# Kernel optimization log

Hardware: AMD Instinct MI355X
Metric: run time of the kernel (lower is better)

Reference implementation:

```python
import jax, jax.numpy as jnp
import numpy as np
from jax.ops import segment_sum, segment_max

N_NODES = 16384
N_EDGES = 262144
NODE_DIM = 480
HIDDEN = 256
OUT_DIM = 128
HEADS = 4
N_GRAPHS = 256


def setup_inputs() -> dict:
    key = jax.random.key(0)
    ks = jax.random.split(key, 40)
    p = {}
    p['x'] = jax.random.normal(ks[0], (N_NODES, NODE_DIM), jnp.float32)
    p['edge_index'] = jax.random.randint(ks[1], (2, N_EDGES), 0, N_NODES)
    p['edge_attr'] = jax.random.uniform(ks[2], (N_EDGES, 1), dtype=jnp.float32)
    p['batch'] = jnp.sort(jax.random.randint(ks[3], (N_NODES,), 0, N_GRAPHS))
    p['num_graphs'] = N_GRAPHS
    def w(k, shape):
        return jax.random.normal(k, shape, jnp.float32) * 0.05
    i = 4
    for l, (din, h, c) in zip((1, 2, 3), [(NODE_DIM, HEADS, HIDDEN // HEADS), (HIDDEN, HEADS, HIDDEN // HEADS), (HIDDEN, 1, OUT_DIM)]):
        dout = h * c
        p[f'Wl{l}'] = w(ks[i], (din, dout)); i += 1
        p[f'bl{l}'] = jnp.zeros((dout,), jnp.float32)
        p[f'Wr{l}'] = w(ks[i], (din, dout)); i += 1
        p[f'br{l}'] = jnp.zeros((dout,), jnp.float32)
        p[f'We{l}'] = w(ks[i], (1, dout)); i += 1
        p[f'att{l}'] = w(ks[i], (h, c)); i += 1
        p[f'bo{l}'] = jnp.zeros((dout,), jnp.float32)
    for l, d in [(1, HIDDEN), (2, HIDDEN), (3, OUT_DIM)]:
        p[f'g{l}'] = jnp.ones((d,), jnp.float32)
        p[f'b{l}'] = jnp.zeros((d,), jnp.float32)
    p['Wres'] = w(ks[i], (NODE_DIM, HIDDEN))
    return p


def _layer_norm(x, g, b):
    mu = x.mean(-1, keepdims=True)
    v = ((x - mu) ** 2).mean(-1, keepdims=True)
    return (x - mu) * jax.lax.rsqrt(v + 1e-5) * g + b


def _gatv2(x, src, dst, ea, Wl, bl, Wr, br, We, att, bias):
    # PyG GATv2Conv, eval mode (dropout off), add_self_loops=True, fill_value='mean'
    N = x.shape[0]
    H, C = att.shape
    # self-loop edge attr = scatter-mean of incoming edge attrs per node
    deg = segment_sum(jnp.ones((src.shape[0],), x.dtype), dst, num_segments=N)
    loop_ea = segment_sum(ea, dst, num_segments=N) / jnp.maximum(deg, 1.0)[:, None]
    ar = jnp.arange(N, dtype=src.dtype)
    src2 = jnp.concatenate([src, ar])
    dst2 = jnp.concatenate([dst, ar])
    ea2 = jnp.concatenate([ea, loop_ea], axis=0)
    xl = (x @ Wl + bl).reshape(N, H, C)
    xr = (x @ Wr + br).reshape(N, H, C)
    e = (ea2 @ We).reshape(-1, H, C)
    m = jax.nn.leaky_relu(xl[src2] + xr[dst2] + e, 0.2)  # [E', H, C]
    alpha = jnp.einsum('ehc,hc->eh', m, att)
    amax = segment_max(alpha, dst2, num_segments=N)  # [N, H]; every node has a self loop
    ex = jnp.exp(alpha - amax[dst2])
    denom = segment_sum(ex, dst2, num_segments=N)
    a = ex / denom[dst2]
    out = segment_sum(a[:, :, None] * xl[src2], dst2, num_segments=N)  # [N, H, C]
    return out.reshape(N, H * C) + bias


def _forward(x, edge_attr, params, edge_index, batch, num_graphs):
    (Wl1, bl1, Wr1, br1, We1, att1, bo1,
     Wl2, bl2, Wr2, br2, We2, att2, bo2,
     Wl3, bl3, Wr3, br3, We3, att3, bo3,
     g1, b1, g2, b2, g3, b3, Wres) = params
    src, dst = edge_index[0], edge_index[1]
    gelu = lambda t: jax.nn.gelu(t, approximate=False)
    h = gelu(_layer_norm(_gatv2(x, src, dst, edge_attr, Wl1, bl1, Wr1, br1, We1, att1, bo1), g1, b1))
    h = h + x @ Wres
    h2 = gelu(_layer_norm(_gatv2(h, src, dst, edge_attr, Wl2, bl2, Wr2, br2, We2, att2, bo2), g2, b2))
    h2 = h2 + h
    h3 = _layer_norm(_gatv2(h2, src, dst, edge_attr, Wl3, bl3, Wr3, br3, We3, att3, bo3), g3, b3)
    # global mean pool over graphs
    sums = segment_sum(h3, batch, num_segments=num_graphs)
    cnt = segment_sum(jnp.ones((h3.shape[0],), h3.dtype), batch, num_segments=num_graphs)
    return sums / jnp.maximum(cnt, 1.0)[:, None]


def reference(x, edge_index, edge_attr, batch, num_graphs,
              Wl1, bl1, Wr1, br1, We1, att1, bo1,
              Wl2, bl2, Wr2, br2, We2, att2, bo2,
              Wl3, bl3, Wr3, br3, We3, att3, bo3,
              g1, b1, g2, b2, g3, b3, Wres):
    params = (Wl1, bl1, Wr1, br1, We1, att1, bo1,
              Wl2, bl2, Wr2, br2, We2, att2, bo2,
              Wl3, bl3, Wr3, br3, We3, att3, bo3,
              g1, b1, g2, b2, g3, b3, Wres)
    return _forward(x, edge_attr, params, edge_index, batch, num_graphs)
```

## Files before the change

kernel.cpp:

```cpp
#include <hip/hip_runtime.h>
#include <hip/hip_bf16.h>
#include <math.h>

#define NN 16384
#define NE 262144
#define KDIM1 480
#define DHID 256
#define DOUT3 128
#define NG 256

typedef short bf16x8 __attribute__((ext_vector_type(8)));
typedef float f32x4 __attribute__((ext_vector_type(4)));

#define LOG2E 1.44269504088896340736f

__device__ __forceinline__ unsigned short f2bf(float f) {
  unsigned u = __float_as_uint(f);
  unsigned r = (u + 0x7fffu + ((u >> 16) & 1u)) >> 16;
  return (unsigned short)r;
}
__device__ __forceinline__ float bf2f(unsigned short u) {
  return __uint_as_float((unsigned)u << 16);
}

__device__ __forceinline__ void gload_lds16(const void* g, void* l) {
  __builtin_amdgcn_global_load_lds((const __attribute__((address_space(1))) void*)g,
                                   (__attribute__((address_space(3))) void*)l,
                                   16, 0, 0);
}


__global__ __launch_bounds__(256) void k_edge_count(const int* __restrict__ ei,
                                                    const float* __restrict__ ea,
                                                    int* __restrict__ deg,
                                                    float* __restrict__ easum) {
  int e = blockIdx.x * 256 + threadIdx.x;
  if (e >= NE) return;
  int d = ei[NE + e];
  atomicAdd(&deg[d], 1);
  atomicAdd(&easum[d], ea[e]);
}

__global__ __launch_bounds__(1024) void k_scan(const int* __restrict__ deg,
                                               float* __restrict__ easum,
                                               int* __restrict__ offs,
                                               int* __restrict__ cursor) {
  __shared__ int sums[1024];
  int t = threadIdx.x;
  int base = t * 16;
  int local[16];
  int s = 0;
#pragma unroll
  for (int i = 0; i < 16; ++i) { local[i] = deg[base + i]; s += local[i]; }
  sums[t] = s;
  __syncthreads();
  for (int d = 1; d < 1024; d <<= 1) {
    int v = (t >= d) ? sums[t - d] : 0;
    __syncthreads();
    sums[t] += v;
    __syncthreads();
  }
  int prefix = (t == 0) ? 0 : sums[t - 1];
#pragma unroll
  for (int i = 0; i < 16; ++i) {
    offs[base + i] = prefix;
    cursor[base + i] = prefix;
    prefix += local[i];
  }
  if (t == 1023) offs[NN] = prefix;
#pragma unroll
  for (int i = 0; i < 16; ++i) {
    easum[base + i] = easum[base + i] / fmaxf((float)local[i], 1.f);
  }
}

__global__ __launch_bounds__(256) void k_fill_csr(const int* __restrict__ ei,
                                                  const float* __restrict__ ea,
                                                  int* __restrict__ cursor,
                                                  int* __restrict__ csr_src,
                                                  float* __restrict__ csr_ea) {
  int e = blockIdx.x * 256 + threadIdx.x;
  if (e >= NE) return;
  int s = ei[e];
  int d = ei[NE + e];
  int pos = atomicAdd(&cursor[d], 1);
  csr_src[pos] = s;
  csr_ea[pos] = ea[e];
}


__global__ __launch_bounds__(256) void k_f32_to_bf16(const float* __restrict__ in,
                                                     unsigned short* __restrict__ out,
                                                     int n) {
  int i = (blockIdx.x * 256 + threadIdx.x) * 4;
  if (i >= n) return;
  float4 v = *(const float4*)&in[i];
  ushort4 o;
  o.x = f2bf(v.x); o.y = f2bf(v.y); o.z = f2bf(v.z); o.w = f2bf(v.w);
  *(ushort4*)&out[i] = o;
}

__global__ __launch_bounds__(256) void k_transpose_bf16(const float* __restrict__ W,
                                                        unsigned short* __restrict__ Wt,
                                                        int K, int N) {
  int idx = blockIdx.x * 256 + threadIdx.x;
  if (idx >= K * N) return;
  int n = idx / K, k = idx % K;
  Wt[idx] = f2bf(W[(size_t)k * N + n]);
}

__global__ __launch_bounds__(256) void k_transpose_lr(const float* __restrict__ Wl,
                                                      const float* __restrict__ Wr,
                                                      unsigned short* __restrict__ Wt,
                                                      int K, int NH) {
  int idx = blockIdx.x * 256 + threadIdx.x;
  if (idx >= 2 * NH * K) return;
  int n = idx / K, k = idx % K;
  float v = (n < NH) ? Wl[(size_t)k * NH + n] : Wr[(size_t)k * NH + (n - NH)];
  Wt[idx] = f2bf(v);
}


#define GEMM_CORE128(A_, Bt_, K_)                                                \
  __shared__ short As[128 * 32];                                                 \
  __shared__ short Bs[128 * 32];                                                 \
  int t = threadIdx.x;                                                           \
  int w = t >> 6;                                                                \
  int lane = t & 63;                                                             \
  int bm = blockIdx.y * 128;                                                     \
  int bn = blockIdx.x * 128;                                                     \
  int wr = w >> 1, wc = w & 1;                                                   \
               \
  const short* Ag0 = A_ + (size_t)(bm + w * 16 + (lane >> 2)) * K_ + (lane & 3) * 8;        \
  const short* Ag1 = A_ + (size_t)(bm + 64 + w * 16 + (lane >> 2)) * K_ + (lane & 3) * 8;   \
  const short* Bg0 = Bt_ + (size_t)(bn + w * 16 + (lane >> 2)) * K_ + (lane & 3) * 8;       \
  const short* Bg1 = Bt_ + (size_t)(bn + 64 + w * 16 + (lane >> 2)) * K_ + (lane & 3) * 8;  \
  short* Al0 = &As[w * 16 * 32];                                                 \
  short* Al1 = &As[(64 + w * 16) * 32];                                          \
  short* Bl0 = &Bs[w * 16 * 32];                                                 \
  short* Bl1 = &Bs[(64 + w * 16) * 32];                                          \
  f32x4 acc[4][4] = {};                                                          \
  for (int k0 = 0; k0 < K_; k0 += 32) {                                          \
    gload_lds16(Ag0, Al0);                                                       \
    gload_lds16(Ag1, Al1);                                                       \
    gload_lds16(Bg0, Bl0);                                                       \
    gload_lds16(Bg1, Bl1);                                                       \
    Ag0 += 32; Ag1 += 32; Bg0 += 32; Bg1 += 32;                                  \
    __syncthreads();                                                             \
    bf16x8 af[4], bf[4];                                                         \
    _Pragma("unroll")                                                            \
    for (int mi = 0; mi < 4; ++mi)                                               \
      af[mi] = *(const bf16x8*)&As[(wr * 64 + mi * 16 + (lane & 15)) * 32 + (lane >> 4) * 8]; \
    _Pragma("unroll")                                                            \
    for (int ni = 0; ni < 4; ++ni)                                               \
      bf[ni] = *(const bf16x8*)&Bs[(wc * 64 + ni * 16 + (lane & 15)) * 32 + (lane >> 4) * 8]; \
    _Pragma("unroll")                                                            \
    for (int mi = 0; mi < 4; ++mi)                                               \
      _Pragma("unroll")                                                          \
      for (int ni = 0; ni < 4; ++ni)                                             \
        acc[mi][ni] = __builtin_amdgcn_mfma_f32_16x16x32_bf16(af[mi], bf[ni], acc[mi][ni], 0, 0, 0); \
    __syncthreads();                                                             \
  }                                                                              \
  int col = lane & 15;                                                           \
  int row4 = (lane >> 4) * 4;

__global__ __launch_bounds__(256) void gemm_lr(const short* __restrict__ A,
                                               const short* __restrict__ Wt,
                                               const float* __restrict__ bl,
                                               const float* __restrict__ br,
                                               unsigned short* __restrict__ xlb,
                                               unsigned short* __restrict__ xrb,
                                               int K, int NH) {
  GEMM_CORE128(A, Wt, K)
  bool right = (bn >= NH);
  unsigned short* outp = right ? xrb : xlb;
  const float* bias = right ? br : bl;
  int cbase = right ? bn - NH : bn;
#pragma unroll
  for (int mi = 0; mi < 4; ++mi) {
#pragma unroll
    for (int ni = 0; ni < 4; ++ni) {
      f32x4 a = acc[mi][ni];
      int gc = cbase + wc * 64 + ni * 16 + col;
      float bv = bias[gc];
#pragma unroll
      for (int r = 0; r < 4; ++r) {
        int gr = bm + wr * 64 + mi * 16 + row4 + r;
        outp[(size_t)gr * NH + gc] = f2bf(a[r] + bv);
      }
    }
  }
}

__global__ __launch_bounds__(256) void gemm_res(const short* __restrict__ A,
                                                const short* __restrict__ Wt,
                                                float* __restrict__ Cf,
                                                unsigned short* __restrict__ outb,
                                                int K, int N) {
  GEMM_CORE128(A, Wt, K)
#pragma unroll
  for (int mi = 0; mi < 4; ++mi) {
#pragma unroll
    for (int ni = 0; ni < 4; ++ni) {
      f32x4 a = acc[mi][ni];
      int gc = bn + wc * 64 + ni * 16 + col;
#pragma unroll
      for (int r = 0; r < 4; ++r) {
        int gr = bm + wr * 64 + mi * 16 + row4 + r;
        size_t o = (size_t)gr * N + gc;
        float v = a[r] + Cf[o];
        Cf[o] = v;
        outb[o] = f2bf(v);
      }
    }
  }
}


template<int D, int H, bool GELU_, bool RES_, bool WF32, bool WBF16>
__global__ __launch_bounds__(256) void gat_fused(
    const unsigned short* __restrict__ xlb, const unsigned short* __restrict__ xrb,
    const float* __restrict__ We, const float* __restrict__ att,
    const float* __restrict__ bo,
    const int* __restrict__ offs, const int* __restrict__ csr_src,
    const float* __restrict__ csr_ea, const float* __restrict__ loop_ea,
    const float* __restrict__ g, const float* __restrict__ bln,
    const float* __restrict__ res,
    float* __restrict__ outf, unsigned short* __restrict__ outb) {
  constexpr int P = D / 64;
  constexpr int C = D / H;
  constexpr int GROUP = C / P;
  int n = (blockIdx.x * blockDim.x + threadIdx.x) >> 6;
  int lane = threadIdx.x & 63;
  if (n >= NN) return;
  int d0 = lane * P;

  float xrv[P], wev[P], attv[P];
  if constexpr (P == 4) {
    ushort4 u = *(const ushort4*)&xrb[(size_t)n * D + d0];
    xrv[0] = bf2f(u.x); xrv[1] = bf2f(u.y); xrv[2] = bf2f(u.z); xrv[3] = bf2f(u.w);
    *(float4*)wev = *(const float4*)&We[d0];
    *(float4*)attv = *(const float4*)&att[d0];
  } else {
    ushort2 u = *(const ushort2*)&xrb[(size_t)n * D + d0];
    xrv[0] = bf2f(u.x); xrv[1] = bf2f(u.y);
    *(float2*)wev = *(const float2*)&We[d0];
    *(float2*)attv = *(const float2*)&att[d0];
  }
#pragma unroll
  for (int p = 0; p < P; ++p) attv[p] *= LOG2E;

#define GATHER(dst, srcidx)                                                  \
  {                                                                          \
    if constexpr (P == 4) {                                                  \
      ushort4 u_ = *(const ushort4*)&xlb[(size_t)(srcidx) * D + d0];         \
      dst[0] = bf2f(u_.x); dst[1] = bf2f(u_.y);                              \
      dst[2] = bf2f(u_.z); dst[3] = bf2f(u_.w);                              \
    } else {                                                                 \
      ushort2 u_ = *(const ushort2*)&xlb[(size_t)(srcidx) * D + d0];         \
      dst[0] = bf2f(u_.x); dst[1] = bf2f(u_.y);                              \
    }                                                                        \
  }

#define ALPHA(out_, xv_, eav_)                                               \
  {                                                                          \
    float partial_ = 0.f;                                                    \
    _Pragma("unroll")                                                        \
    for (int p = 0; p < P; ++p) {                                            \
      float s_ = xv_[p] + xrv[p] + (eav_) * wev[p];                          \
      s_ = fmaxf(s_, 0.2f * s_);                                             \
      partial_ = fmaf(s_, attv[p], partial_);                                \
    }                                                                        \
    _Pragma("unroll")                                                        \
    for (int w_ = 1; w_ < GROUP; w_ <<= 1) partial_ += __shfl_xor(partial_, w_, 64); \
    out_ = partial_;                                                         \
  }

  float acc[P];
  float xs[P];
  GATHER(xs, n)
  float m;
  ALPHA(m, xs, loop_ea[n])
  float l = 1.f;
#pragma unroll
  for (int p = 0; p < P; ++p) acc[p] = xs[p];

  int beg = offs[n];
  int cnt = offs[n + 1] - beg;
  int sbeg = __builtin_amdgcn_readfirstlane(beg);
  int scnt = __builtin_amdgcn_readfirstlane(cnt);

  int e = 0;
  for (; e + 2 <= scnt; e += 2) {
    int src0 = csr_src[sbeg + e];
    int src1 = csr_src[sbeg + e + 1];
    float ea0 = csr_ea[sbeg + e];
    float ea1 = csr_ea[sbeg + e + 1];
    float xv0[P], xv1[P];
    GATHER(xv0, src0)
    GATHER(xv1, src1)
    float a0, a1;
    ALPHA(a0, xv0, ea0)
    ALPHA(a1, xv1, ea1)
    float nm = fmaxf(m, fmaxf(a0, a1));
    float sc = exp2f(m - nm);
    float pe0 = exp2f(a0 - nm);
    float pe1 = exp2f(a1 - nm);
    l = fmaf(l, sc, pe0 + pe1);
#pragma unroll
    for (int p = 0; p < P; ++p)
      acc[p] = fmaf(acc[p], sc, fmaf(pe0, xv0[p], pe1 * xv1[p]));
    m = nm;
  }
  if (e < scnt) {
    int src0 = csr_src[sbeg + e];
    float ea0 = csr_ea[sbeg + e];
    float xv0[P];
    GATHER(xv0, src0)
    float a0;
    ALPHA(a0, xv0, ea0)
    float nm = fmaxf(m, a0);
    float sc = exp2f(m - nm);
    float pe0 = exp2f(a0 - nm);
    l = fmaf(l, sc, pe0);
#pragma unroll
    for (int p = 0; p < P; ++p) acc[p] = fmaf(acc[p], sc, pe0 * xv0[p]);
    m = nm;
  }
#undef GATHER
#undef ALPHA

  float inv = 1.f / l;
  float y[P];
#pragma unroll
  for (int p = 0; p < P; ++p) y[p] = fmaf(acc[p], inv, bo[d0 + p]);

  float s = 0.f, s2 = 0.f;
#pragma unroll
  for (int p = 0; p < P; ++p) { s += y[p]; s2 = fmaf(y[p], y[p], s2); }
#pragma unroll
  for (int w = 1; w < 64; w <<= 1) {
    s += __shfl_xor(s, w, 64);
    s2 += __shfl_xor(s2, w, 64);
  }
  float mu = s * (1.f / D);
  float var = s2 * (1.f / D) - mu * mu;
  float rr = rsqrtf(var + 1e-5f);

  float z[P];
#pragma unroll
  for (int p = 0; p < P; ++p) {
    float v = (y[p] - mu) * rr * g[d0 + p] + bln[d0 + p];
    if (GELU_) v = 0.5f * v * (1.f + erff(v * 0.70710678118654752f));
    if (RES_) v += res[(size_t)n * D + d0 + p];
    z[p] = v;
  }
  if (WF32) {
    float* orow = outf + (size_t)n * D;
    if constexpr (P == 4) *(float4*)&orow[d0] = *(float4*)z;
    else                  *(float2*)&orow[d0] = *(float2*)z;
  }
  if (WBF16) {
    unsigned short* orow = outb + (size_t)n * D;
    if constexpr (P == 4) {
      ushort4 o; o.x = f2bf(z[0]); o.y = f2bf(z[1]); o.z = f2bf(z[2]); o.w = f2bf(z[3]);
      *(ushort4*)&orow[d0] = o;
    } else {
      ushort2 o; o.x = f2bf(z[0]); o.y = f2bf(z[1]);
      *(ushort2*)&orow[d0] = o;
    }
  }
}


__device__ __forceinline__ int lower_bound_i(const int* arr, int n, int val) {
  int lo = 0, hi = n;
  while (lo < hi) {
    int mid = (lo + hi) >> 1;
    if (arr[mid] < val) lo = mid + 1; else hi = mid;
  }
  return lo;
}

__global__ __launch_bounds__(128) void k_pool(const float* __restrict__ h3,
                                              const int* __restrict__ batch,
                                              float* __restrict__ out) {
  int gidx = blockIdx.x;
  int d = threadIdx.x;
  int lo = lower_bound_i(batch, NN, gidx);
  int hi = lower_bound_i(batch, NN, gidx + 1);
  float s = 0.f;
  for (int n = lo; n < hi; ++n) s += h3[(size_t)n * DOUT3 + d];
  int cnt = hi - lo;
  out[gidx * DOUT3 + d] = s / fmaxf((float)cnt, 1.f);
}


extern "C" void kernel_launch(void* const* d_in, const int* in_sizes, int n_in,
                              void* d_out, int out_size, void* d_ws, size_t ws_size,
                              hipStream_t stream) {
  const float* x   = (const float*)d_in[0];
  const int*   ei  = (const int*)d_in[1];
  const float* ea  = (const float*)d_in[2];
  const int*   bat = (const int*)d_in[3];
  const float* Wl1 = (const float*)d_in[5];  const float* bl1 = (const float*)d_in[6];
  const float* Wr1 = (const float*)d_in[7];  const float* br1 = (const float*)d_in[8];
  const float* We1 = (const float*)d_in[9];  const float* at1 = (const float*)d_in[10];
  const float* bo1 = (const float*)d_in[11];
  const float* Wl2 = (const float*)d_in[12]; const float* bl2 = (const float*)d_in[13];
  const float* Wr2 = (const float*)d_in[14]; const float* br2 = (const float*)d_in[15];
  const float* We2 = (const float*)d_in[16]; const float* at2 = (const float*)d_in[17];
  const float* bo2 = (const float*)d_in[18];
  const float* Wl3 = (const float*)d_in[19]; const float* bl3 = (const float*)d_in[20];
  const float* Wr3 = (const float*)d_in[21]; const float* br3 = (const float*)d_in[22];
  const float* We3 = (const float*)d_in[23]; const float* at3 = (const float*)d_in[24];
  const float* bo3 = (const float*)d_in[25];
  const float* g1 = (const float*)d_in[26]; const float* b1 = (const float*)d_in[27];
  const float* g2 = (const float*)d_in[28]; const float* b2 = (const float*)d_in[29];
  const float* g3 = (const float*)d_in[30]; const float* b3 = (const float*)d_in[31];
  const float* Wres = (const float*)d_in[32];
  float* out = (float*)d_out;

  char* ws = (char*)d_ws;
  size_t off = 0;
  unsigned short* xlb = (unsigned short*)(ws + off); off += (size_t)NN * DHID * 2;
  unsigned short* xrb = (unsigned short*)(ws + off); off += (size_t)NN * DHID * 2;
  float* hb = (float*)(ws + off); off += (size_t)NN * DHID * 4;
  float* h3 = (float*)(ws + off); off += (size_t)NN * DOUT3 * 4;
  unsigned short* actb0 = (unsigned short*)(ws + off); off += (size_t)NN * KDIM1 * 2;
  unsigned short* actb1 = (unsigned short*)(ws + off); off += (size_t)NN * DHID * 2;
  int*   deg    = (int*)(ws + off); off += NN * 4;
  int*   offs   = (int*)(ws + off); off += (NN + 1) * 4 + 60;
  int*   cursor = (int*)(ws + off); off += NN * 4;
  float* easum  = (float*)(ws + off); off += NN * 4;
  int*   csr_src = (int*)(ws + off); off += (size_t)NE * 4;
  float* csr_ea  = (float*)(ws + off); off += (size_t)NE * 4;
  unsigned short* Wc1 = (unsigned short*)(ws + off); off += (size_t)2 * DHID * KDIM1 * 2;
  unsigned short* Wrs = (unsigned short*)(ws + off); off += (size_t)DHID * KDIM1 * 2;
  unsigned short* Wc2 = (unsigned short*)(ws + off); off += (size_t)2 * DHID * DHID * 2;
  unsigned short* Wc3 = (unsigned short*)(ws + off); off += (size_t)2 * DOUT3 * DHID * 2;

  hipMemsetAsync(deg, 0, NN * 4, stream);
  hipMemsetAsync(easum, 0, NN * 4, stream);
  k_edge_count<<<NE / 256, 256, 0, stream>>>(ei, ea, deg, easum);
  k_scan<<<1, 1024, 0, stream>>>(deg, easum, offs, cursor);
  k_fill_csr<<<NE / 256, 256, 0, stream>>>(ei, ea, cursor, csr_src, csr_ea);

  k_f32_to_bf16<<<(NN * KDIM1 / 4 + 255) / 256, 256, 0, stream>>>(x, actb0, NN * KDIM1);
  k_transpose_lr<<<(2 * DHID * KDIM1 + 255) / 256, 256, 0, stream>>>(Wl1, Wr1, Wc1, KDIM1, DHID);
  k_transpose_bf16<<<(DHID * KDIM1 + 255) / 256, 256, 0, stream>>>(Wres, Wrs, KDIM1, DHID);
  k_transpose_lr<<<(2 * DHID * DHID + 255) / 256, 256, 0, stream>>>(Wl2, Wr2, Wc2, DHID, DHID);
  k_transpose_lr<<<(2 * DOUT3 * DHID + 255) / 256, 256, 0, stream>>>(Wl3, Wr3, Wc3, DHID, DOUT3);

  dim3 blk(256);
  int nwave_blocks = NN / 4;

  gemm_lr<<<dim3(2 * DHID / 128, NN / 128), blk, 0, stream>>>(
      (const short*)actb0, (const short*)Wc1, bl1, br1, xlb, xrb, KDIM1, DHID);
  gat_fused<DHID, 4, true, false, true, false><<<nwave_blocks, blk, 0, stream>>>(
      xlb, xrb, We1, at1, bo1, offs, csr_src, csr_ea, easum, g1, b1, nullptr, hb, nullptr);
  gemm_res<<<dim3(DHID / 128, NN / 128), blk, 0, stream>>>(
      (const short*)actb0, (const short*)Wrs, hb, actb1, KDIM1, DHID);

  gemm_lr<<<dim3(2 * DHID / 128, NN / 128), blk, 0, stream>>>(
      (const short*)actb1, (const short*)Wc2, bl2, br2, xlb, xrb, DHID, DHID);
  gat_fused<DHID, 4, true, true, false, true><<<nwave_blocks, blk, 0, stream>>>(
      xlb, xrb, We2, at2, bo2, offs, csr_src, csr_ea, easum, g2, b2, hb, nullptr, actb1);

  gemm_lr<<<dim3(2 * DOUT3 / 128, NN / 128), blk, 0, stream>>>(
      (const short*)actb1, (const short*)Wc3, bl3, br3, xlb, xrb, DHID, DOUT3);
  gat_fused<DOUT3, 1, false, false, true, false><<<nwave_blocks, blk, 0, stream>>>(
      xlb, xrb, We3, at3, bo3, offs, csr_src, csr_ea, easum, g3, b3, nullptr, h3, nullptr);

  k_pool<<<NG, 128, 0, stream>>>(h3, bat, out);
}
```

Measured before the change: 274.7 us.

## Use persistent atomic work queue in GAT kernels, unroll edges by four, fuse prep kernels

The GAT aggregation kernels become persistent: 2048 blocks pull node indices from a global atomic counter instead of launching one wave per node, which is meant to balance the uneven per-node degrees. The edge loop is unrolled from two to four edges per iteration to keep more gathers in flight. The five input conversion and weight-transpose kernels are merged into one prep launch, and the two memsets become one that also clears the queue counters. The trade-off is one atomic per node and coarser tail behaviour.

```diff
diff --git a/kernel.cpp b/kernel.cpp
--- a/kernel.cpp
+++ b/kernel.cpp
@@ -89,35 +89,57 @@
 }
 
 
-__global__ __launch_bounds__(256) void k_f32_to_bf16(const float* __restrict__ in,
-                                                     unsigned short* __restrict__ out,
-                                                     int n) {
-  int i = (blockIdx.x * 256 + threadIdx.x) * 4;
-  if (i >= n) return;
-  float4 v = *(const float4*)&in[i];
-  ushort4 o;
-  o.x = f2bf(v.x); o.y = f2bf(v.y); o.z = f2bf(v.z); o.w = f2bf(v.w);
-  *(ushort4*)&out[i] = o;
-}
-
-__global__ __launch_bounds__(256) void k_transpose_bf16(const float* __restrict__ W,
-                                                        unsigned short* __restrict__ Wt,
-                                                        int K, int N) {
+#define PREP_S0 (NN * KDIM1 / 4)
+#define PREP_S1 (2 * DHID * KDIM1)
+#define PREP_S2 (DHID * KDIM1)
+#define PREP_S3 (2 * DHID * DHID)
+#define PREP_S4 (2 * DOUT3 * DHID)
+#define PREP_TOTAL (PREP_S0 + PREP_S1 + PREP_S2 + PREP_S3 + PREP_S4)
+
+__global__ __launch_bounds__(256) void k_prep(
+    const float* __restrict__ x,
+    const float* __restrict__ Wl1, const float* __restrict__ Wr1,
+    const float* __restrict__ Wres,
+    const float* __restrict__ Wl2, const float* __restrict__ Wr2,
+    const float* __restrict__ Wl3, const float* __restrict__ Wr3,
+    unsigned short* __restrict__ actb0, unsigned short* __restrict__ Wc1,
+    unsigned short* __restrict__ Wrs, unsigned short* __restrict__ Wc2,
+    unsigned short* __restrict__ Wc3) {
   int idx = blockIdx.x * 256 + threadIdx.x;
-  if (idx >= K * N) return;
-  int n = idx / K, k = idx % K;
-  Wt[idx] = f2bf(W[(size_t)k * N + n]);
-}
-
-__global__ __launch_bounds__(256) void k_transpose_lr(const float* __restrict__ Wl,
-                                                      const float* __restrict__ Wr,
-                                                      unsigned short* __restrict__ Wt,
-                                                      int K, int NH) {
-  int idx = blockIdx.x * 256 + threadIdx.x;
-  if (idx >= 2 * NH * K) return;
-  int n = idx / K, k = idx % K;
-  float v = (n < NH) ? Wl[(size_t)k * NH + n] : Wr[(size_t)k * NH + (n - NH)];
-  Wt[idx] = f2bf(v);
+  if (idx < PREP_S0) {
+    int i = idx * 4;
+    float4 v = *(const float4*)&x[i];
+    ushort4 o;
+    o.x = f2bf(v.x); o.y = f2bf(v.y); o.z = f2bf(v.z); o.w = f2bf(v.w);
+    *(ushort4*)&actb0[i] = o;
+    return;
+  }
+  idx -= PREP_S0;
+  if (idx < PREP_S1) {
+    int n = idx / KDIM1, k = idx % KDIM1;
+    float v = (n < DHID) ? Wl1[(size_t)k * DHID + n] : Wr1[(size_t)k * DHID + (n - DHID)];
+    Wc1[idx] = f2bf(v);
+    return;
+  }
+  idx -= PREP_S1;
+  if (idx < PREP_S2) {
+    int n = idx / KDIM1, k = idx % KDIM1;
+    Wrs[idx] = f2bf(Wres[(size_t)k * DHID + n]);
+    return;
+  }
+  idx -= PREP_S2;
+  if (idx < PREP_S3) {
+    int n = idx / DHID, k = idx % DHID;
+    float v = (n < DHID) ? Wl2[(size_t)k * DHID + n] : Wr2[(size_t)k * DHID + (n - DHID)];
+    Wc2[idx] = f2bf(v);
+    return;
+  }
+  idx -= PREP_S3;
+  if (idx < PREP_S4) {
+    int n = idx / DHID, k = idx % DHID;
+    float v = (n < DOUT3) ? Wl3[(size_t)k * DOUT3 + n] : Wr3[(size_t)k * DOUT3 + (n - DOUT3)];
+    Wc3[idx] = f2bf(v);
+  }
 }
 
 
@@ -130,7 +152,6 @@
   int bm = blockIdx.y * 128;                                                     \
   int bn = blockIdx.x * 128;                                                     \
   int wr = w >> 1, wc = w & 1;                                                   \
-               \
   const short* Ag0 = A_ + (size_t)(bm + w * 16 + (lane >> 2)) * K_ + (lane & 3) * 8;        \
   const short* Ag1 = A_ + (size_t)(bm + 64 + w * 16 + (lane >> 2)) * K_ + (lane & 3) * 8;   \
   const short* Bg0 = Bt_ + (size_t)(bn + w * 16 + (lane >> 2)) * K_ + (lane & 3) * 8;       \
@@ -147,18 +168,18 @@
     gload_lds16(Bg1, Bl1);                                                       \
     Ag0 += 32; Ag1 += 32; Bg0 += 32; Bg1 += 32;                                  \
     __syncthreads();                                                             \
-    bf16x8 af[4], bf[4];                                                         \
+    bf16x8 af[4], bfv[4];                                                        \
     _Pragma("unroll")                                                            \
     for (int mi = 0; mi < 4; ++mi)                                               \
       af[mi] = *(const bf16x8*)&As[(wr * 64 + mi * 16 + (lane & 15)) * 32 + (lane >> 4) * 8]; \
     _Pragma("unroll")                                                            \
     for (int ni = 0; ni < 4; ++ni)                                               \
-      bf[ni] = *(const bf16x8*)&Bs[(wc * 64 + ni * 16 + (lane & 15)) * 32 + (lane >> 4) * 8]; \
+      bfv[ni] = *(const bf16x8*)&Bs[(wc * 64 + ni * 16 + (lane & 15)) * 32 + (lane >> 4) * 8]; \
     _Pragma("unroll")                                                            \
     for (int mi = 0; mi < 4; ++mi)                                               \
       _Pragma("unroll")                                                          \
       for (int ni = 0; ni < 4; ++ni)                                             \
-        acc[mi][ni] = __builtin_amdgcn_mfma_f32_16x16x32_bf16(af[mi], bf[ni], acc[mi][ni], 0, 0, 0); \
+        acc[mi][ni] = __builtin_amdgcn_mfma_f32_16x16x32_bf16(af[mi], bfv[ni], acc[mi][ni], 0, 0, 0); \
     __syncthreads();                                                             \
   }                                                                              \
   int col = lane & 15;                                                           \
@@ -226,24 +247,19 @@
     const float* __restrict__ csr_ea, const float* __restrict__ loop_ea,
     const float* __restrict__ g, const float* __restrict__ bln,
     const float* __restrict__ res,
-    float* __restrict__ outf, unsigned short* __restrict__ outb) {
+    float* __restrict__ outf, unsigned short* __restrict__ outb,
+    int* __restrict__ gcnt) {
   constexpr int P = D / 64;
   constexpr int C = D / H;
   constexpr int GROUP = C / P;
-  int n = (blockIdx.x * blockDim.x + threadIdx.x) >> 6;
   int lane = threadIdx.x & 63;
-  if (n >= NN) return;
   int d0 = lane * P;
 
-  float xrv[P], wev[P], attv[P];
+  float wev[P], attv[P];
   if constexpr (P == 4) {
-    ushort4 u = *(const ushort4*)&xrb[(size_t)n * D + d0];
-    xrv[0] = bf2f(u.x); xrv[1] = bf2f(u.y); xrv[2] = bf2f(u.z); xrv[3] = bf2f(u.w);
     *(float4*)wev = *(const float4*)&We[d0];
     *(float4*)attv = *(const float4*)&att[d0];
   } else {
-    ushort2 u = *(const ushort2*)&xrb[(size_t)n * D + d0];
-    xrv[0] = bf2f(u.x); xrv[1] = bf2f(u.y);
     *(float2*)wev = *(const float2*)&We[d0];
     *(float2*)attv = *(const float2*)&att[d0];
   }
@@ -276,100 +292,127 @@
     out_ = partial_;                                                         \
   }
 
-  float acc[P];
-  float xs[P];
-  GATHER(xs, n)
-  float m;
-  ALPHA(m, xs, loop_ea[n])
-  float l = 1.f;
-#pragma unroll
-  for (int p = 0; p < P; ++p) acc[p] = xs[p];
-
-  int beg = offs[n];
-  int cnt = offs[n + 1] - beg;
-  int sbeg = __builtin_amdgcn_readfirstlane(beg);
-  int scnt = __builtin_amdgcn_readfirstlane(cnt);
-
-  int e = 0;
-  for (; e + 2 <= scnt; e += 2) {
-    int src0 = csr_src[sbeg + e];
-    int src1 = csr_src[sbeg + e + 1];
-    float ea0 = csr_ea[sbeg + e];
-    float ea1 = csr_ea[sbeg + e + 1];
-    float xv0[P], xv1[P];
-    GATHER(xv0, src0)
-    GATHER(xv1, src1)
-    float a0, a1;
-    ALPHA(a0, xv0, ea0)
-    ALPHA(a1, xv1, ea1)
-    float nm = fmaxf(m, fmaxf(a0, a1));
-    float sc = exp2f(m - nm);
-    float pe0 = exp2f(a0 - nm);
-    float pe1 = exp2f(a1 - nm);
-    l = fmaf(l, sc, pe0 + pe1);
-#pragma unroll
-    for (int p = 0; p < P; ++p)
-      acc[p] = fmaf(acc[p], sc, fmaf(pe0, xv0[p], pe1 * xv1[p]));
-    m = nm;
-  }
-  if (e < scnt) {
-    int src0 = csr_src[sbeg + e];
-    float ea0 = csr_ea[sbeg + e];
-    float xv0[P];
-    GATHER(xv0, src0)
-    float a0;
-    ALPHA(a0, xv0, ea0)
-    float nm = fmaxf(m, a0);
-    float sc = exp2f(m - nm);
-    float pe0 = exp2f(a0 - nm);
-    l = fmaf(l, sc, pe0);
-#pragma unroll
-    for (int p = 0; p < P; ++p) acc[p] = fmaf(acc[p], sc, pe0 * xv0[p]);
-    m = nm;
+  for (;;) {
+    int n;
+    if (lane == 0) n = atomicAdd(gcnt, 1);
+    n = __shfl(n, 0, 64);
+    if (n >= NN) break;
+
+    float xrv[P];
+    if constexpr (P == 4) {
+      ushort4 u = *(const ushort4*)&xrb[(size_t)n * D + d0];
+      xrv[0] = bf2f(u.x); xrv[1] = bf2f(u.y); xrv[2] = bf2f(u.z); xrv[3] = bf2f(u.w);
+    } else {
+      ushort2 u = *(const ushort2*)&xrb[(size_t)n * D + d0];
+      xrv[0] = bf2f(u.x); xrv[1] = bf2f(u.y);
+    }
+
+    float acc[P];
+    float xs[P];
+    GATHER(xs, n)
+    float m;
+    ALPHA(m, xs, loop_ea[n])
+    float l = 1.f;
+#pragma unroll
+    for (int p = 0; p < P; ++p) acc[p] = xs[p];
+
+    int beg = offs[n];
+    int cnt = offs[n + 1] - beg;
+    int sbeg = __builtin_amdgcn_readfirstlane(beg);
+    int scnt = __builtin_amdgcn_readfirstlane(cnt);
+
+    int e = 0;
+    for (; e + 4 <= scnt; e += 4) {
+      int src0 = csr_src[sbeg + e];
+      int src1 = csr_src[sbeg + e + 1];
+      int src2 = csr_src[sbeg + e + 2];
+      int src3 = csr_src[sbeg + e + 3];
+      float ea0 = csr_ea[sbeg + e];
+      float ea1 = csr_ea[sbeg + e + 1];
+      float ea2 = csr_ea[sbeg + e + 2];
+      float ea3 = csr_ea[sbeg + e + 3];
+      float xv0[P], xv1[P], xv2[P], xv3[P];
+      GATHER(xv0, src0)
+      GATHER(xv1, src1)
+      GATHER(xv2, src2)
+      GATHER(xv3, src3)
+      float a0, a1, a2, a3;
+      ALPHA(a0, xv0, ea0)
+      ALPHA(a1, xv1, ea1)
+      ALPHA(a2, xv2, ea2)
+      ALPHA(a3, xv3, ea3)
+      float nm = fmaxf(fmaxf(m, fmaxf(a0, a1)), fmaxf(a2, a3));
+      float sc = exp2f(m - nm);
+      float pe0 = exp2f(a0 - nm);
+      float pe1 = exp2f(a1 - nm);
+      float pe2 = exp2f(a2 - nm);
+      float pe3 = exp2f(a3 - nm);
+      l = fmaf(l, sc, (pe0 + pe1) + (pe2 + pe3));
+#pragma unroll
+      for (int p = 0; p < P; ++p)
+        acc[p] = fmaf(acc[p], sc,
+                      fmaf(pe0, xv0[p], fmaf(pe1, xv1[p], fmaf(pe2, xv2[p], pe3 * xv3[p]))));
+      m = nm;
+    }
+    for (; e < scnt; ++e) {
+      int src0 = csr_src[sbeg + e];
+      float ea0 = csr_ea[sbeg + e];
+      float xv0[P];
+      GATHER(xv0, src0)
+      float a0;
+      ALPHA(a0, xv0, ea0)
+      float nm = fmaxf(m, a0);
+      float sc = exp2f(m - nm);
+      float pe0 = exp2f(a0 - nm);
+      l = fmaf(l, sc, pe0);
+#pragma unroll
+      for (int p = 0; p < P; ++p) acc[p] = fmaf(acc[p], sc, pe0 * xv0[p]);
+      m = nm;
+    }
+
+    float inv = 1.f / l;
+    float y[P];
+#pragma unroll
+    for (int p = 0; p < P; ++p) y[p] = fmaf(acc[p], inv, bo[d0 + p]);
+
+    float s = 0.f, s2 = 0.f;
+#pragma unroll
+    for (int p = 0; p < P; ++p) { s += y[p]; s2 = fmaf(y[p], y[p], s2); }
+#pragma unroll
+    for (int w = 1; w < 64; w <<= 1) {
+      s += __shfl_xor(s, w, 64);
+      s2 += __shfl_xor(s2, w, 64);
+    }
+    float mu = s * (1.f / D);
+    float var = s2 * (1.f / D) - mu * mu;
+    float rr = rsqrtf(var + 1e-5f);
+
+    float z[P];
+#pragma unroll
+    for (int p = 0; p < P; ++p) {
+      float v = (y[p] - mu) * rr * g[d0 + p] + bln[d0 + p];
+      if (GELU_) v = 0.5f * v * (1.f + erff(v * 0.70710678118654752f));
+      if (RES_) v += res[(size_t)n * D + d0 + p];
+      z[p] = v;
+    }
+    if (WF32) {
+      float* orow = outf + (size_t)n * D;
+      if constexpr (P == 4) *(float4*)&orow[d0] = *(float4*)z;
+      else                  *(float2*)&orow[d0] = *(float2*)z;
+    }
+    if (WBF16) {
+      unsigned short* orow = outb + (size_t)n * D;
+      if constexpr (P == 4) {
+        ushort4 o; o.x = f2bf(z[0]); o.y = f2bf(z[1]); o.z = f2bf(z[2]); o.w = f2bf(z[3]);
+        *(ushort4*)&orow[d0] = o;
+      } else {
+        ushort2 o; o.x = f2bf(z[0]); o.y = f2bf(z[1]);
+        *(ushort2*)&orow[d0] = o;
+      }
+    }
   }
 #undef GATHER
 #undef ALPHA
-
-  float inv = 1.f / l;
-  float y[P];
-#pragma unroll
-  for (int p = 0; p < P; ++p) y[p] = fmaf(acc[p], inv, bo[d0 + p]);
-
-  float s = 0.f, s2 = 0.f;
-#pragma unroll
-  for (int p = 0; p < P; ++p) { s += y[p]; s2 = fmaf(y[p], y[p], s2); }
-#pragma unroll
-  for (int w = 1; w < 64; w <<= 1) {
-    s += __shfl_xor(s, w, 64);
-    s2 += __shfl_xor(s2, w, 64);
-  }
-  float mu = s * (1.f / D);
-  float var = s2 * (1.f / D) - mu * mu;
-  float rr = rsqrtf(var + 1e-5f);
-
-  float z[P];
-#pragma unroll
-  for (int p = 0; p < P; ++p) {
-    float v = (y[p] - mu) * rr * g[d0 + p] + bln[d0 + p];
-    if (GELU_) v = 0.5f * v * (1.f + erff(v * 0.70710678118654752f));
-    if (RES_) v += res[(size_t)n * D + d0 + p];
-    z[p] = v;
-  }
-  if (WF32) {
-    float* orow = outf + (size_t)n * D;
-    if constexpr (P == 4) *(float4*)&orow[d0] = *(float4*)z;
-    else                  *(float2*)&orow[d0] = *(float2*)z;
-  }
-  if (WBF16) {
-    unsigned short* orow = outb + (size_t)n * D;
-    if constexpr (P == 4) {
-      ushort4 o; o.x = f2bf(z[0]); o.y = f2bf(z[1]); o.z = f2bf(z[2]); o.w = f2bf(z[3]);
-      *(ushort4*)&orow[d0] = o;
-    } else {
-      ushort2 o; o.x = f2bf(z[0]); o.y = f2bf(z[1]);
-      *(ushort2*)&orow[d0] = o;
-    }
-  }
 }
 
 
@@ -423,16 +466,18 @@
 
   char* ws = (char*)d_ws;
   size_t off = 0;
+  int*   deg    = (int*)(ws + off); off += NN * 4;
+  float* easum  = (float*)(ws + off); off += NN * 4;
+  int*   gcnt   = (int*)(ws + off); off += 16;
+  size_t zero_bytes = off;
   unsigned short* xlb = (unsigned short*)(ws + off); off += (size_t)NN * DHID * 2;
   unsigned short* xrb = (unsigned short*)(ws + off); off += (size_t)NN * DHID * 2;
   float* hb = (float*)(ws + off); off += (size_t)NN * DHID * 4;
   float* h3 = (float*)(ws + off); off += (size_t)NN * DOUT3 * 4;
   unsigned short* actb0 = (unsigned short*)(ws + off); off += (size_t)NN * KDIM1 * 2;
   unsigned short* actb1 = (unsigned short*)(ws + off); off += (size_t)NN * DHID * 2;
-  int*   deg    = (int*)(ws + off); off += NN * 4;
   int*   offs   = (int*)(ws + off); off += (NN + 1) * 4 + 60;
   int*   cursor = (int*)(ws + off); off += NN * 4;
-  float* easum  = (float*)(ws + off); off += NN * 4;
   int*   csr_src = (int*)(ws + off); off += (size_t)NE * 4;
   float* csr_ea  = (float*)(ws + off); off += (size_t)NE * 4;
   unsigned short* Wc1 = (unsigned short*)(ws + off); off += (size_t)2 * DHID * KDIM1 * 2;
@@ -440,37 +485,32 @@
   unsigned short* Wc2 = (unsigned short*)(ws + off); off += (size_t)2 * DHID * DHID * 2;
   unsigned short* Wc3 = (unsigned short*)(ws + off); off += (size_t)2 * DOUT3 * DHID * 2;
 
-  hipMemsetAsync(deg, 0, NN * 4, stream);
-  hipMemsetAsync(easum, 0, NN * 4, stream);
+  hipMemsetAsync(deg, 0, zero_bytes, stream);
   k_edge_count<<<NE / 256, 256, 0, stream>>>(ei, ea, deg, easum);
   k_scan<<<1, 1024, 0, stream>>>(deg, easum, offs, cursor);
   k_fill_csr<<<NE / 256, 256, 0, stream>>>(ei, ea, cursor, csr_src, csr_ea);
-
-  k_f32_to_bf16<<<(NN * KDIM1 / 4 + 255) / 256, 256, 0, stream>>>(x, actb0, NN * KDIM1);
-  k_transpose_lr<<<(2 * DHID * KDIM1 + 255) / 256, 256, 0, stream>>>(Wl1, Wr1, Wc1, KDIM1, DHID);
-  k_transpose_bf16<<<(DHID * KDIM1 + 255) / 256, 256, 0, stream>>>(Wres, Wrs, KDIM1, DHID);
-  k_transpose_lr<<<(2 * DHID * DHID + 255) / 256, 256, 0, stream>>>(Wl2, Wr2, Wc2, DHID, DHID);
-  k_transpose_lr<<<(2 * DOUT3 * DHID + 255) / 256, 256, 0, stream>>>(Wl3, Wr3, Wc3, DHID, DOUT3);
+  k_prep<<<PREP_TOTAL / 256, 256, 0, stream>>>(x, Wl1, Wr1, Wres, Wl2, Wr2, Wl3, Wr3,
+                                               actb0, Wc1, Wrs, Wc2, Wc3);
 
   dim3 blk(256);
-  int nwave_blocks = NN / 4;
+  int gat_blocks = 2048;
 
   gemm_lr<<<dim3(2 * DHID / 128, NN / 128), blk, 0, stream>>>(
       (const short*)actb0, (const short*)Wc1, bl1, br1, xlb, xrb, KDIM1, DHID);
-  gat_fused<DHID, 4, true, false, true, false><<<nwave_blocks, blk, 0, stream>>>(
-      xlb, xrb, We1, at1, bo1, offs, csr_src, csr_ea, easum, g1, b1, nullptr, hb, nullptr);
+  gat_fused<DHID, 4, true, false, true, false><<<gat_blocks, blk, 0, stream>>>(
+      xlb, xrb, We1, at1, bo1, offs, csr_src, csr_ea, easum, g1, b1, nullptr, hb, nullptr, gcnt + 0);
   gemm_res<<<dim3(DHID / 128, NN / 128), blk, 0, stream>>>(
       (const short*)actb0, (const short*)Wrs, hb, actb1, KDIM1, DHID);
 
   gemm_lr<<<dim3(2 * DHID / 128, NN / 128), blk, 0, stream>>>(
       (const short*)actb1, (const short*)Wc2, bl2, br2, xlb, xrb, DHID, DHID);
-  gat_fused<DHID, 4, true, true, false, true><<<nwave_blocks, blk, 0, stream>>>(
-      xlb, xrb, We2, at2, bo2, offs, csr_src, csr_ea, easum, g2, b2, hb, nullptr, actb1);
+  gat_fused<DHID, 4, true, true, false, true><<<gat_blocks, blk, 0, stream>>>(
+      xlb, xrb, We2, at2, bo2, offs, csr_src, csr_ea, easum, g2, b2, hb, nullptr, actb1, gcnt + 1);
 
   gemm_lr<<<dim3(2 * DOUT3 / 128, NN / 128), blk, 0, stream>>>(
       (const short*)actb1, (const short*)Wc3, bl3, br3, xlb, xrb, DHID, DOUT3);
-  gat_fused<DOUT3, 1, false, false, true, false><<<nwave_blocks, blk, 0, stream>>>(
-      xlb, xrb, We3, at3, bo3, offs, csr_src, csr_ea, easum, g3, b3, nullptr, h3, nullptr);
+  gat_fused<DOUT3, 1, false, false, true, false><<<gat_blocks, blk, 0, stream>>>(
+      xlb, xrb, We3, at3, bo3, offs, csr_src, csr_ea, easum, g3, b3, nullptr, h3, nullptr, gcnt + 2);
 
   k_pool<<<NG, 128, 0, stream>>>(h3, bat, out);
 }
```

Measured after the change: 1.047 ms. +281.2%, slower.
